# Kernel tuning notes

Hardware: AMD Instinct MI355X
Metric: run time of the kernel (lower is better)

Reference implementation:

```python
import jax, jax.numpy as jnp
import numpy as np

N, D, H, E = 4096, 512, 8, 131072
DH = D // H
EPS = 1e-5
NEG = -1e9


def layer_norm(x, w, b):
    m = jnp.mean(x, axis=-1, keepdims=True)
    v = jnp.mean((x - m) ** 2, axis=-1, keepdims=True)
    return (x - m) * jax.lax.rsqrt(v + EPS) * w + b


def setup_inputs() -> dict:
    key = jax.random.key(0)
    ks = jax.random.split(key, 10)
    s = 0.02
    return {
        "x": jax.random.normal(ks[0], (N, D), dtype=jnp.float32),
        "edge_index": jax.random.randint(ks[1], (2, E), 0, N, dtype=jnp.int64),
        "ln1_w": jnp.ones((D,), jnp.float32),
        "ln1_b": jnp.zeros((D,), jnp.float32),
        "w_in": jax.random.normal(ks[2], (3 * D, D), jnp.float32) * s,
        "b_in": jnp.zeros((3 * D,), jnp.float32),
        "w_out": jax.random.normal(ks[3], (D, D), jnp.float32) * s,
        "b_out": jnp.zeros((D,), jnp.float32),
        "ln2_w": jnp.ones((D,), jnp.float32),
        "ln2_b": jnp.zeros((D,), jnp.float32),
        "w1": jax.random.normal(ks[4], (4 * D, D), jnp.float32) * s,
        "b1": jnp.zeros((4 * D,), jnp.float32),
        "w2": jax.random.normal(ks[5], (D, 4 * D), jnp.float32) * s,
        "b2": jnp.zeros((D,), jnp.float32),
    }


def reference(x, edge_index, ln1_w, ln1_b, w_in, b_in, w_out, b_out,
              ln2_w, ln2_b, w1, b1, w2, b2):
    n = x.shape[0]
    # adjacency mask: allowed where edge exists or on diagonal
    adj = jnp.zeros((n, n), dtype=bool)
    adj = adj.at[edge_index[0], edge_index[1]].set(True)
    adj = adj.at[jnp.arange(n), jnp.arange(n)].set(True)
    add_mask = jnp.where(adj, 0.0, NEG).astype(x.dtype)  # [n, n]

    xn = layer_norm(x, ln1_w, ln1_b)
    qkv = xn @ w_in.T + b_in  # [n, 3D]
    q, k, v = jnp.split(qkv, 3, axis=-1)
    # [n, D] -> [H, n, DH]
    q = q.reshape(n, H, DH).transpose(1, 0, 2)
    k = k.reshape(n, H, DH).transpose(1, 0, 2)
    v = v.reshape(n, H, DH).transpose(1, 0, 2)
    scores = jnp.einsum("hqd,hkd->hqk", q, k) / jnp.sqrt(jnp.asarray(DH, x.dtype))
    scores = scores + add_mask[None]
    attn = jax.nn.softmax(scores, axis=-1)
    o = jnp.einsum("hqk,hkd->hqd", attn, v)  # [H, n, DH]
    o = o.transpose(1, 0, 2).reshape(n, D)
    attn_out = o @ w_out.T + b_out

    x = x + attn_out  # residual (dropout=0 / eval)
    xm = layer_norm(x, ln2_w, ln2_b)
    mlp = jax.nn.relu(xm @ w1.T + b1) @ w2.T + b2
    return x + mlp
```

## Files before the change

kernel.cpp:

```cpp
#include <hip/hip_runtime.h>

#define NN 4096
#define DD 512
#define HH 8
#define DHH 64

typedef __attribute__((ext_vector_type(8))) __bf16 bfrag;
typedef __attribute__((ext_vector_type(8))) short short8;
typedef __attribute__((ext_vector_type(8))) unsigned short ushort8v;
typedef __attribute__((ext_vector_type(4))) float f32x4;
typedef unsigned int uint32;

#define GLOAD16(gp, lp)                                                        \
    __builtin_amdgcn_global_load_lds(                                          \
        (const __attribute__((address_space(1))) unsigned int*)(gp),           \
        (__attribute__((address_space(3))) unsigned int*)(lp), 16, 0, 0)

template <int N>
__device__ __forceinline__ void waitcnt_vm() {
    if constexpr (N == 0) asm volatile("s_waitcnt vmcnt(0)" ::: "memory");
    else if constexpr (N == 4) asm volatile("s_waitcnt vmcnt(4)" ::: "memory");
    else if constexpr (N == 6) asm volatile("s_waitcnt vmcnt(6)" ::: "memory");
    else if constexpr (N == 8) asm volatile("s_waitcnt vmcnt(8)" ::: "memory");
    else static_assert(N == 0, "unsupported vmcnt literal");
}

__device__ __forceinline__ unsigned short f2b(float f) {
    unsigned int u = __builtin_bit_cast(unsigned int, f);
    unsigned int r = 0x7fffu + ((u >> 16) & 1u);
    return (unsigned short)((u + r) >> 16);
}

__device__ __forceinline__ float b2f(unsigned short u) {
    return __builtin_bit_cast(float, (unsigned int)u << 16);
}

__device__ __forceinline__ float fexp2(float x) {
#if __has_builtin(__builtin_amdgcn_exp2f)
    return __builtin_amdgcn_exp2f(x);
#else
    return exp2f(x);
#endif
}

__device__ __forceinline__ void load_edge(const void* ei, int E, int i, int is32,
                                          int& r, int& c) {
    if (is32) {
        const int* p = (const int*)ei;
        r = p[i]; c = p[E + i];
    } else {
        const long long* p = (const long long*)ei;
        r = (int)p[i]; c = (int)p[E + i];
    }
}

__device__ __forceinline__ void ln_row_wave(const float* __restrict__ x,
                                            const float* __restrict__ w,
                                            const float* __restrict__ b,
                                            unsigned short* __restrict__ out,
                                            int row, int lane) {
    const float4* xp = reinterpret_cast<const float4*>(x + (size_t)row * DD + lane * 8);
    const float4 v0 = xp[0], v1 = xp[1];
    float s  = (v0.x + v0.y) + (v0.z + v0.w) + (v1.x + v1.y) + (v1.z + v1.w);
    float s2 = v0.x * v0.x + v0.y * v0.y + v0.z * v0.z + v0.w * v0.w +
               v1.x * v1.x + v1.y * v1.y + v1.z * v1.z + v1.w * v1.w;
#pragma unroll
    for (int d = 1; d < 64; d <<= 1) {
        s += __shfl_xor(s, d);
        s2 += __shfl_xor(s2, d);
    }
    const float mean = s * (1.f / DD);
    const float var = fmaxf(s2 * (1.f / DD) - mean * mean, 0.f);
    const float rs = rsqrtf(var + 1e-5f);
    const float4* wp = reinterpret_cast<const float4*>(w + lane * 8);
    const float4* bp = reinterpret_cast<const float4*>(b + lane * 8);
    const float4 w0 = wp[0], w1 = wp[1], b0 = bp[0], b1 = bp[1];
    ushort8v o;
    o[0] = f2b((v0.x - mean) * rs * w0.x + b0.x);
    o[1] = f2b((v0.y - mean) * rs * w0.y + b0.y);
    o[2] = f2b((v0.z - mean) * rs * w0.z + b0.z);
    o[3] = f2b((v0.w - mean) * rs * w0.w + b0.w);
    o[4] = f2b((v1.x - mean) * rs * w1.x + b1.x);
    o[5] = f2b((v1.y - mean) * rs * w1.y + b1.y);
    o[6] = f2b((v1.z - mean) * rs * w1.z + b1.z);
    o[7] = f2b((v1.w - mean) * rs * w1.w + b1.w);
    *reinterpret_cast<ushort8v*>(out + (size_t)row * DD + lane * 8) = o;
}

__global__ __launch_bounds__(256) void ln_rows(const float* __restrict__ x,
                                               const float* __restrict__ w,
                                               const float* __restrict__ b,
                                               unsigned short* __restrict__ out) {
    ln_row_wave(x, w, b, out, blockIdx.x * 4 + (threadIdx.x >> 6), threadIdx.x & 63);
}

#define W_IN_N 786432
#define W_OUT_N 262144
#define W1_N 1048576
#define W2_N 1048576
#define CVT_BLKS 3072
#define LN_BLKS 1024
__global__ __launch_bounds__(256) void prologue(
    const float* __restrict__ w_in, const float* __restrict__ w_out,
    const float* __restrict__ w1, const float* __restrict__ w2,
    unsigned short* __restrict__ o_in, unsigned short* __restrict__ o_out,
    unsigned short* __restrict__ o1, unsigned short* __restrict__ o2,
    const float* __restrict__ x, const float* __restrict__ ln1w,
    const float* __restrict__ ln1b, unsigned short* __restrict__ xn,
    const void* __restrict__ ei, uint32* __restrict__ mask, int E) {
    const int bb = blockIdx.x;
    if (bb < CVT_BLKS) {
        int idx = (bb * 256 + threadIdx.x) * 4;
        const float* src;
        unsigned short* dst;
        int off;
        if (idx < W_IN_N) { src = w_in; dst = o_in; off = idx; }
        else if (idx < W_IN_N + W_OUT_N) { src = w_out; dst = o_out; off = idx - W_IN_N; }
        else if (idx < W_IN_N + W_OUT_N + W1_N) { src = w1; dst = o1; off = idx - (W_IN_N + W_OUT_N); }
        else { src = w2; dst = o2; off = idx - (W_IN_N + W_OUT_N + W1_N); }
        float4 v = *reinterpret_cast<const float4*>(src + off);
        ushort4 o;
        o.x = f2b(v.x); o.y = f2b(v.y); o.z = f2b(v.z); o.w = f2b(v.w);
        *reinterpret_cast<ushort4*>(dst + off) = o;
    } else if (bb < CVT_BLKS + LN_BLKS) {
        ln_row_wave(x, ln1w, ln1b, xn,
                    (bb - CVT_BLKS) * 4 + (threadIdx.x >> 6), threadIdx.x & 63);
    } else {
        __shared__ int s_any;
        if (threadIdx.x == 0) s_any = 0;
        __syncthreads();
        if (((const int*)ei)[2 * threadIdx.x + 1] != 0) atomicOr(&s_any, 1);
        __syncthreads();
        const int is32 = s_any;
        const int tid = (bb - (CVT_BLKS + LN_BLKS)) * 256 + threadIdx.x;
        const int total = E + NN;
        if (tid < total) {
            int r, c;
            if (tid < E) load_edge(ei, E, tid, is32, r, c);
            else { r = tid - E; c = r; }
            atomicOr(&mask[r * 128 + (c >> 5)], 1u << (c & 31));
        }
    }
}

template <int BM, int BN, int EPI>
__global__ __launch_bounds__(256) void gemm_swz(const unsigned short* __restrict__ A,
                                                const unsigned short* __restrict__ B,
                                                int K,
                                                const float* __restrict__ bias,
                                                const float* __restrict__ resid,
                                                float* __restrict__ out_f,
                                                unsigned short* __restrict__ out_b,
                                                float* __restrict__ q_out,
                                                unsigned short* __restrict__ k_out,
                                                unsigned short* __restrict__ v_out) {
    constexpr int MR = BM / 32;
    constexpr int NR = BN / 32;
    constexpr int LA = BM / 32;
    constexpr int LB = BN / 32;
    __shared__ __align__(16) unsigned short a_lds[2 * BM * 64];
    __shared__ __align__(16) unsigned short b_lds[2 * BN * 64];
    const int tid = threadIdx.x;
    const int lane = tid & 63;
    const int wave = tid >> 6;
    const int wm = wave >> 1, wn = wave & 1;
    const int wgid = blockIdx.x;
    const int tm = wgid % (NN / BM);
    const int tn = wgid / (NN / BM);

    f32x4 acc[MR][NR];
#pragma unroll
    for (int mi = 0; mi < MR; ++mi)
#pragma unroll
        for (int ni = 0; ni < NR; ++ni) acc[mi][ni] = (f32x4){0.f, 0.f, 0.f, 0.f};

    const int srow = lane >> 3;
    const int sswz = ((lane & 7) ^ srow) << 3;
    const unsigned short* a_src = A + (size_t)(tm * BM + srow) * K + sswz;
    const unsigned short* b_src = B + (size_t)(tn * BN + srow) * K + sswz;

    auto stage = [&](int k0, int buf) {
        unsigned short* al = a_lds + buf * (BM * 64);
        unsigned short* bl = b_lds + buf * (BN * 64);
#pragma unroll
        for (int i = 0; i < LA; ++i) {
            const int c = wave * LA + i;
            GLOAD16(a_src + (size_t)c * 8 * K + k0, al + c * 512);
        }
#pragma unroll
        for (int i = 0; i < LB; ++i) {
            const int c = wave * LB + i;
            GLOAD16(b_src + (size_t)c * 8 * K + k0, bl + c * 512);
        }
    };

    stage(0, 0);
    const int NT = K >> 6;
    for (int t = 0; t < NT; ++t) {
        const int cur = t & 1;
        if (t + 1 < NT) {
            stage((t + 1) << 6, cur ^ 1);
            waitcnt_vm<LA + LB>();
        } else {
            waitcnt_vm<0>();
        }
        __builtin_amdgcn_s_barrier();
        asm volatile("" ::: "memory");
        const unsigned short* al = a_lds + cur * (BM * 64);
        const unsigned short* bl = b_lds + cur * (BN * 64);
#pragma unroll
        for (int ks = 0; ks < 2; ++ks) {
            const int cswz = (((lane >> 4) + ks * 4) ^ (lane & 7)) << 3;
            const int rl = lane & 15;
            bfrag af[MR], bfr[NR];
#pragma unroll
            for (int mi = 0; mi < MR; ++mi)
                af[mi] = *reinterpret_cast<const bfrag*>(
                    &al[(wm * (BM / 2) + mi * 16 + rl) * 64 + cswz]);
#pragma unroll
            for (int ni = 0; ni < NR; ++ni)
                bfr[ni] = *reinterpret_cast<const bfrag*>(
                    &bl[(wn * (BN / 2) + ni * 16 + rl) * 64 + cswz]);
#pragma unroll
            for (int mi = 0; mi < MR; ++mi)
#pragma unroll
                for (int ni = 0; ni < NR; ++ni)
                    acc[mi][ni] = __builtin_amdgcn_mfma_f32_16x16x32_bf16(
                        af[mi], bfr[ni], acc[mi][ni], 0, 0, 0);
        }
        asm volatile("" ::: "memory");
        __builtin_amdgcn_s_barrier();
    }

    const int r0 = (lane >> 4) << 2;
    const int cl = lane & 15;
#pragma unroll
    for (int mi = 0; mi < MR; ++mi) {
#pragma unroll
        for (int ni = 0; ni < NR; ++ni) {
#pragma unroll
            for (int r = 0; r < 4; ++r) {
                int gr = tm * BM + wm * (BM / 2) + mi * 16 + r0 + r;
                int gc = tn * BN + wn * (BN / 2) + ni * 16 + cl;
                float v = acc[mi][ni][r] + bias[gc];
                if (EPI == 0) {
                    if (gc < 512) {
                        q_out[(size_t)gr * 512 + gc] = v * 0.18033688011112042f;
                    } else if (gc < 1024) {
                        k_out[(size_t)gr * 512 + (gc - 512)] = f2b(v);
                    } else {
                        v_out[(size_t)gr * 512 + (gc - 1024)] = f2b(v);
                    }
                } else if (EPI == 1) {
                    out_f[(size_t)gr * 512 + gc] =
                        v + resid[(size_t)gr * 512 + gc];
                } else {
                    out_b[(size_t)gr * 2048 + gc] = f2b(fmaxf(v, 0.f));
                }
            }
        }
    }
}

__global__ __launch_bounds__(256) void attn_sparse(const float* __restrict__ qf,
                                                   const unsigned short* __restrict__ kb,
                                                   const unsigned short* __restrict__ vb,
                                                   const uint32* __restrict__ mask,
                                                   unsigned short* __restrict__ o_buf) {
    __shared__ int s_cols[4][1024];
    __shared__ int s_cnt[4];
    const int lane = threadIdx.x & 63;
    const int wid = threadIdx.x >> 6;
    const int q = blockIdx.x * 4 + wid;

    if (lane == 0) s_cnt[wid] = 0;
    uint32 w0 = mask[q * 128 + lane];
    uint32 w1 = mask[q * 128 + 64 + lane];
    const int base0 = lane * 32, base1 = (64 + lane) * 32;
    while (w0) {
        int b = __builtin_ctz(w0);
        w0 &= w0 - 1;
        int pos = atomicAdd(&s_cnt[wid], 1);
        s_cols[wid][pos & 1023] = base0 + b;
    }
    while (w1) {
        int b = __builtin_ctz(w1);
        w1 &= w1 - 1;
        int pos = atomicAdd(&s_cnt[wid], 1);
        s_cols[wid][pos & 1023] = base1 + b;
    }
    const int cnt = min(s_cnt[wid], 1024);

    const float4* qp = reinterpret_cast<const float4*>(qf + (size_t)q * DD + lane * 8);
    const float4 q0 = qp[0], q1 = qp[1];

    float m_run = -3.0e38f, l_run = 0.f;
    float oa[8];
#pragma unroll
    for (int i = 0; i < 8; ++i) oa[i] = 0.f;

    for (int j0 = 0; j0 < cnt; j0 += 8) {
        float s_arr[8];
        int col_arr[8];
#pragma unroll
        for (int u = 0; u < 8; ++u) {
            const int idx = j0 + u;
            const bool act = idx < cnt;
            const int col = s_cols[wid][act ? idx : 0];
            col_arr[u] = col;
            ushort8v kq = *reinterpret_cast<const ushort8v*>(
                kb + (size_t)col * DD + lane * 8);
            float d = q0.x * b2f(kq[0]);
            d = fmaf(q0.y, b2f(kq[1]), d);
            d = fmaf(q0.z, b2f(kq[2]), d);
            d = fmaf(q0.w, b2f(kq[3]), d);
            d = fmaf(q1.x, b2f(kq[4]), d);
            d = fmaf(q1.y, b2f(kq[5]), d);
            d = fmaf(q1.z, b2f(kq[6]), d);
            d = fmaf(q1.w, b2f(kq[7]), d);
            d += __shfl_xor(d, 1);
            d += __shfl_xor(d, 2);
            d += __shfl_xor(d, 4);
            s_arr[u] = act ? d : -3.0e38f;
        }
        float mloc = fmaxf(fmaxf(fmaxf(s_arr[0], s_arr[1]), fmaxf(s_arr[2], s_arr[3])),
                           fmaxf(fmaxf(s_arr[4], s_arr[5]), fmaxf(s_arr[6], s_arr[7])));
        if (mloc > m_run) {
            const float alpha = fexp2(m_run - mloc);
            l_run *= alpha;
#pragma unroll
            for (int i = 0; i < 8; ++i) oa[i] *= alpha;
            m_run = mloc;
        }
#pragma unroll
        for (int u = 0; u < 8; ++u) {
            const float p = fexp2(s_arr[u] - m_run);
            l_run += p;
            ushort8v vq = *reinterpret_cast<const ushort8v*>(
                vb + (size_t)col_arr[u] * DD + lane * 8);
#pragma unroll
            for (int i = 0; i < 8; ++i) oa[i] = fmaf(p, b2f(vq[i]), oa[i]);
        }
    }

    const float rl = 1.f / l_run;
    ushort8v ov;
#pragma unroll
    for (int i = 0; i < 8; ++i) ov[i] = f2b(oa[i] * rl);
    *reinterpret_cast<ushort8v*>(o_buf + (size_t)q * DD + lane * 8) = ov;
}

extern "C" void kernel_launch(void* const* d_in, const int* in_sizes, int n_in,
                              void* d_out, int out_size, void* d_ws, size_t ws_size,
                              hipStream_t stream) {
    const float* x = (const float*)d_in[0];
    const void* ei = d_in[1];
    const float* ln1w = (const float*)d_in[2];
    const float* ln1b = (const float*)d_in[3];
    const float* w_in = (const float*)d_in[4];
    const float* b_in = (const float*)d_in[5];
    const float* w_out = (const float*)d_in[6];
    const float* b_out = (const float*)d_in[7];
    const float* ln2w = (const float*)d_in[8];
    const float* ln2b = (const float*)d_in[9];
    const float* w1 = (const float*)d_in[10];
    const float* b1 = (const float*)d_in[11];
    const float* w2 = (const float*)d_in[12];
    const float* b2 = (const float*)d_in[13];
    float* out = (float*)d_out;
    const int E = in_sizes[1] / 2;

    char* ws = (char*)d_ws;
    size_t off = 0;
    auto alloc = [&](size_t bytes) -> void* {
        void* p = ws + off;
        off = (off + bytes + 255) & ~(size_t)255;
        return p;
    };
    uint32* mask1 = (uint32*)alloc((size_t)NN * 128 * 4);
    unsigned short* w_in_b = (unsigned short*)alloc((size_t)1536 * 512 * 2);
    unsigned short* w_out_b = (unsigned short*)alloc((size_t)512 * 512 * 2);
    unsigned short* w1_b = (unsigned short*)alloc((size_t)2048 * 512 * 2);
    unsigned short* w2_b = (unsigned short*)alloc((size_t)512 * 2048 * 2);
    unsigned short* xn = (unsigned short*)alloc((size_t)NN * DD * 2);
    float* q_f = (float*)alloc((size_t)NN * DD * 4);
    unsigned short* k_b = (unsigned short*)alloc((size_t)NN * DD * 2);
    unsigned short* v_b = (unsigned short*)alloc((size_t)NN * DD * 2);
    unsigned short* o_buf = (unsigned short*)alloc((size_t)NN * DD * 2);
    float* x1 = (float*)alloc((size_t)NN * DD * 4);
    unsigned short* xm = (unsigned short*)alloc((size_t)NN * DD * 2);
    unsigned short* h_buf = (unsigned short*)q_f;

    hipMemsetAsync(mask1, 0, (size_t)NN * 128 * 4, stream);

    const int adj_blks = (E + NN + 255) / 256;
    prologue<<<CVT_BLKS + LN_BLKS + adj_blks, 256, 0, stream>>>(
        w_in, w_out, w1, w2, w_in_b, w_out_b, w1_b, w2_b,
        x, ln1w, ln1b, xn, ei, mask1, E);

    gemm_swz<128, 64, 0><<<32 * 24, 256, 0, stream>>>(
        xn, w_in_b, 512, b_in, nullptr, nullptr, nullptr, q_f, k_b, v_b);
    attn_sparse<<<NN / 4, 256, 0, stream>>>(q_f, k_b, v_b, mask1, o_buf);
    gemm_swz<64, 64, 1><<<64 * 8, 256, 0, stream>>>(
        o_buf, w_out_b, 512, b_out, x, x1, nullptr, nullptr, nullptr, nullptr);
    ln_rows<<<NN / 4, 256, 0, stream>>>(x1, ln2w, ln2b, xm);
    gemm_swz<128, 128, 2><<<32 * 16, 256, 0, stream>>>(
        xm, w1_b, 512, b1, nullptr, nullptr, h_buf, nullptr, nullptr, nullptr);
    gemm_swz<64, 64, 1><<<64 * 8, 256, 0, stream>>>(
        h_buf, w2_b, 2048, b2, x1, out, nullptr, nullptr, nullptr, nullptr);
}
```

Measured before the change: 106.1 us.

## Split-K out-projection and FFN2 GEMMs with atomic accumulation into pre-seeded residual buffers

The LayerNorm passes now pre-seed x1 with x+b_out and out with x1+b2. The out-projection and second MLP GEMMs then use split-K, atomically adding partial products into those buffers instead of reading the residual in their epilogue. FFN2 also moves from 64x64 tiles to 128x128 tiles split four ways along K, and out-proj is split two ways for more blocks. This raises parallelism on the K=2048 GEMM and drops the residual read, at the cost of float atomic traffic and non-deterministic summation order.

```diff
diff --git a/kernel.cpp b/kernel.cpp
--- a/kernel.cpp
+++ b/kernel.cpp
@@ -58,6 +58,8 @@
                                             const float* __restrict__ w,
                                             const float* __restrict__ b,
                                             unsigned short* __restrict__ out,
+                                            float* __restrict__ seed_dst,
+                                            const float* __restrict__ seed_b,
                                             int row, int lane) {
     const float4* xp = reinterpret_cast<const float4*>(x + (size_t)row * DD + lane * 8);
     const float4 v0 = xp[0], v1 = xp[1];
@@ -85,13 +87,24 @@
     o[6] = f2b((v1.z - mean) * rs * w1.z + b1.z);
     o[7] = f2b((v1.w - mean) * rs * w1.w + b1.w);
     *reinterpret_cast<ushort8v*>(out + (size_t)row * DD + lane * 8) = o;
+    if (seed_dst) {
+        const float4* sp = reinterpret_cast<const float4*>(seed_b + lane * 8);
+        const float4 sb0 = sp[0], sb1 = sp[1];
+        float4 o0 = {v0.x + sb0.x, v0.y + sb0.y, v0.z + sb0.z, v0.w + sb0.w};
+        float4 o1 = {v1.x + sb1.x, v1.y + sb1.y, v1.z + sb1.z, v1.w + sb1.w};
+        float4* dp = reinterpret_cast<float4*>(seed_dst + (size_t)row * DD + lane * 8);
+        dp[0] = o0; dp[1] = o1;
+    }
 }
 
 __global__ __launch_bounds__(256) void ln_rows(const float* __restrict__ x,
                                                const float* __restrict__ w,
                                                const float* __restrict__ b,
-                                               unsigned short* __restrict__ out) {
-    ln_row_wave(x, w, b, out, blockIdx.x * 4 + (threadIdx.x >> 6), threadIdx.x & 63);
+                                               unsigned short* __restrict__ out,
+                                               float* __restrict__ seed_dst,
+                                               const float* __restrict__ seed_b) {
+    ln_row_wave(x, w, b, out, seed_dst, seed_b,
+                blockIdx.x * 4 + (threadIdx.x >> 6), threadIdx.x & 63);
 }
 
 #define W_IN_N 786432
@@ -107,6 +120,7 @@
     unsigned short* __restrict__ o1, unsigned short* __restrict__ o2,
     const float* __restrict__ x, const float* __restrict__ ln1w,
     const float* __restrict__ ln1b, unsigned short* __restrict__ xn,
+    float* __restrict__ x1_seed, const float* __restrict__ b_out,
     const void* __restrict__ ei, uint32* __restrict__ mask, int E) {
     const int bb = blockIdx.x;
     if (bb < CVT_BLKS) {
@@ -123,7 +137,7 @@
         o.x = f2b(v.x); o.y = f2b(v.y); o.z = f2b(v.z); o.w = f2b(v.w);
         *reinterpret_cast<ushort4*>(dst + off) = o;
     } else if (bb < CVT_BLKS + LN_BLKS) {
-        ln_row_wave(x, ln1w, ln1b, xn,
+        ln_row_wave(x, ln1w, ln1b, xn, x1_seed, b_out,
                     (bb - CVT_BLKS) * 4 + (threadIdx.x >> 6), threadIdx.x & 63);
     } else {
         __shared__ int s_any;
@@ -143,12 +157,11 @@
     }
 }
 
-template <int BM, int BN, int EPI>
+template <int BM, int BN, int SPLITK, int EPI>
 __global__ __launch_bounds__(256) void gemm_swz(const unsigned short* __restrict__ A,
                                                 const unsigned short* __restrict__ B,
                                                 int K,
                                                 const float* __restrict__ bias,
-                                                const float* __restrict__ resid,
                                                 float* __restrict__ out_f,
                                                 unsigned short* __restrict__ out_b,
                                                 float* __restrict__ q_out,
@@ -164,9 +177,14 @@
     const int lane = tid & 63;
     const int wave = tid >> 6;
     const int wm = wave >> 1, wn = wave & 1;
+    constexpr int nm = NN / BM;
     const int wgid = blockIdx.x;
-    const int tm = wgid % (NN / BM);
-    const int tn = wgid / (NN / BM);
+    const int id = wgid % (nm * SPLITK);
+    const int tm = id % nm;
+    const int slice = id / nm;
+    const int tn = wgid / (nm * SPLITK);
+    const int Ksl = K / SPLITK;
+    const int kbase = slice * Ksl;
 
     f32x4 acc[MR][NR];
 #pragma unroll
@@ -176,8 +194,8 @@
 
     const int srow = lane >> 3;
     const int sswz = ((lane & 7) ^ srow) << 3;
-    const unsigned short* a_src = A + (size_t)(tm * BM + srow) * K + sswz;
-    const unsigned short* b_src = B + (size_t)(tn * BN + srow) * K + sswz;
+    const unsigned short* a_src = A + (size_t)(tm * BM + srow) * K + kbase + sswz;
+    const unsigned short* b_src = B + (size_t)(tn * BN + srow) * K + kbase + sswz;
 
     auto stage = [&](int k0, int buf) {
         unsigned short* al = a_lds + buf * (BM * 64);
@@ -195,7 +213,7 @@
     };
 
     stage(0, 0);
-    const int NT = K >> 6;
+    const int NT = Ksl >> 6;
     for (int t = 0; t < NT; ++t) {
         const int cur = t & 1;
         if (t + 1 < NT) {
@@ -242,8 +260,9 @@
             for (int r = 0; r < 4; ++r) {
                 int gr = tm * BM + wm * (BM / 2) + mi * 16 + r0 + r;
                 int gc = tn * BN + wn * (BN / 2) + ni * 16 + cl;
-                float v = acc[mi][ni][r] + bias[gc];
-                if (EPI == 0) {
+                float v = acc[mi][ni][r];
+                if constexpr (EPI != 3) v += bias[gc];
+                if constexpr (EPI == 0) {
                     if (gc < 512) {
                         q_out[(size_t)gr * 512 + gc] = v * 0.18033688011112042f;
                     } else if (gc < 1024) {
@@ -251,11 +270,10 @@
                     } else {
                         v_out[(size_t)gr * 512 + (gc - 1024)] = f2b(v);
                     }
-                } else if (EPI == 1) {
-                    out_f[(size_t)gr * 512 + gc] =
-                        v + resid[(size_t)gr * 512 + gc];
+                } else if constexpr (EPI == 2) {
+                    out_b[(size_t)gr * 2048 + gc] = f2b(fmaxf(v, 0.f));
                 } else {
-                    out_b[(size_t)gr * 2048 + gc] = f2b(fmaxf(v, 0.f));
+                    unsafeAtomicAdd(&out_f[(size_t)gr * 512 + gc], v);
                 }
             }
         }
@@ -396,16 +414,16 @@
     const int adj_blks = (E + NN + 255) / 256;
     prologue<<<CVT_BLKS + LN_BLKS + adj_blks, 256, 0, stream>>>(
         w_in, w_out, w1, w2, w_in_b, w_out_b, w1_b, w2_b,
-        x, ln1w, ln1b, xn, ei, mask1, E);
-
-    gemm_swz<128, 64, 0><<<32 * 24, 256, 0, stream>>>(
-        xn, w_in_b, 512, b_in, nullptr, nullptr, nullptr, q_f, k_b, v_b);
+        x, ln1w, ln1b, xn, x1, b_out, ei, mask1, E);
+
+    gemm_swz<128, 64, 1, 0><<<32 * 24, 256, 0, stream>>>(
+        xn, w_in_b, 512, b_in, nullptr, nullptr, q_f, k_b, v_b);
     attn_sparse<<<NN / 4, 256, 0, stream>>>(q_f, k_b, v_b, mask1, o_buf);
-    gemm_swz<64, 64, 1><<<64 * 8, 256, 0, stream>>>(
-        o_buf, w_out_b, 512, b_out, x, x1, nullptr, nullptr, nullptr, nullptr);
-    ln_rows<<<NN / 4, 256, 0, stream>>>(x1, ln2w, ln2b, xm);
-    gemm_swz<128, 128, 2><<<32 * 16, 256, 0, stream>>>(
-        xm, w1_b, 512, b1, nullptr, nullptr, h_buf, nullptr, nullptr, nullptr);
-    gemm_swz<64, 64, 1><<<64 * 8, 256, 0, stream>>>(
-        h_buf, w2_b, 2048, b2, x1, out, nullptr, nullptr, nullptr, nullptr);
-}
+    gemm_swz<64, 64, 2, 3><<<64 * 2 * 8, 256, 0, stream>>>(
+        o_buf, w_out_b, 512, nullptr, x1, nullptr, nullptr, nullptr, nullptr);
+    ln_rows<<<NN / 4, 256, 0, stream>>>(x1, ln2w, ln2b, xm, out, b2);
+    gemm_swz<128, 128, 1, 2><<<32 * 16, 256, 0, stream>>>(
+        xm, w1_b, 512, b1, nullptr, h_buf, nullptr, nullptr, nullptr);
+    gemm_swz<128, 128, 4, 3><<<32 * 4 * 4, 256, 0, stream>>>(
+        h_buf, w2_b, 2048, nullptr, out, nullptr, nullptr, nullptr, nullptr);
+}
```

After: 128.2 us. +20.9%, slower.
